# Performance work log

Hardware: AMD Instinct MI355X
Metric: run time of the kernel (lower is better)

Reference implementation:

```python
import jax, jax.numpy as jnp
import numpy as np

BETA = 0.95
THRESH = 1.0
SLOPE = 25.0  # fast_sigmoid surrogate slope

@jax.custom_vjp
def spike(u):
    # Heaviside forward, fast-sigmoid surrogate backward (snntorch.surrogate.fast_sigmoid)
    return (u > 0).astype(u.dtype)

def _spike_fwd(u):
    return spike(u), u

def _spike_bwd(u, g):
    return (g / (SLOPE * jnp.abs(u) + 1.0) ** 2,)

spike.defvjp(_spike_fwd, _spike_bwd)

def setup_inputs() -> dict:
    key = jax.random.key(0)
    ks = jax.random.split(key, 7)
    B, T, D_in, D_h, D_out = 4096, 5, 1024, 4096, 1024
    def lin(kw, kb, fan_in, fan_out):
        bound = 1.0 / np.sqrt(fan_in)
        W = jax.random.uniform(kw, (fan_out, fan_in), jnp.float32, -bound, bound)
        b = jax.random.uniform(kb, (fan_out,), jnp.float32, -bound, bound)
        return W, b
    W1, b1 = lin(ks[0], ks[1], D_in, D_h)
    W2, b2 = lin(ks[2], ks[3], D_h, D_h)
    W3, b3 = lin(ks[4], ks[5], D_h, D_out)
    x = jax.random.normal(ks[6], (B, T, D_in), jnp.float32)
    return {"x": x, "W1": W1, "b1": b1, "W2": W2, "b2": b2, "W3": W3, "b3": b3}

def _lif(cur, mem, spk_prev):
    # snnTorch Leaky, reset_mechanism='subtract': reset uses previous step's (detached) spike
    mem = BETA * mem + cur - jax.lax.stop_gradient(spk_prev) * THRESH
    spk = spike(mem - THRESH)
    return spk, mem

def reference(x, W1, b1, W2, b2, W3, b3):
    B = x.shape[0]
    Dh, Do = W2.shape[0], W3.shape[0]
    z = jnp.zeros((B, Dh), x.dtype)
    zo = jnp.zeros((B, Do), x.dtype)
    init = (z, z, zo, z, z, zo)  # mem1, mem2, mem3, spk1, spk2, spk3

    def step(carry, x_t):
        mem1, mem2, mem3, s1, s2, s3 = carry
        s1, mem1 = _lif(x_t @ W1.T + b1, mem1, s1)
        s2, mem2 = _lif(s1 @ W2.T + b2, mem2, s2)
        s3, mem3 = _lif(s2 @ W3.T + b3, mem3, s3)
        return (mem1, mem2, mem3, s1, s2, s3), s3

    xt = jnp.swapaxes(x, 0, 1)  # [T, B, D_in]
    _, spk3_rec = jax.lax.scan(step, init, xt)
    return spk3_rec.sum(axis=0)  # [B, D_out]
```

## Files before the change

### kernel.cpp

```cpp
#include <hip/hip_runtime.h>
#include <stdint.h>

typedef __attribute__((ext_vector_type(8))) short  short8;
typedef __attribute__((ext_vector_type(4))) float  f32x4;

static constexpr float BETA = 0.95f;
static constexpr unsigned ROWCAP = 64;

__device__ __forceinline__ unsigned short f2bf(float f) {
  uint32_t u = __float_as_uint(f);
  uint32_t r = (u + 0x7fffu + ((u >> 16) & 1u)) >> 16;
  return (unsigned short)r;
}
__device__ __forceinline__ float bf2f(unsigned short s) {
  return __uint_as_float((uint32_t)s << 16);
}

__device__ __forceinline__ void gload16(const void* g, void* l) {
  __builtin_amdgcn_global_load_lds(
      (const __attribute__((address_space(1))) uint32_t*)g,
      (__attribute__((address_space(3))) uint32_t*)l, 16, 0, 0);
}

__global__ void cvt_xt_k(const float* __restrict__ x, unsigned short* __restrict__ xbt, int t) {
  int i = blockIdx.x * blockDim.x + threadIdx.x;
  int k8 = i & 127, b = i >> 7;
  const f32x4* s = (const f32x4*)(x + ((size_t)b * 5 + t) * 1024 + (size_t)k8 * 8);
  f32x4 a = s[0], c = s[1];
  short8 o;
#pragma unroll
  for (int j = 0; j < 4; ++j) { o[j] = (short)f2bf(a[j]); o[4 + j] = (short)f2bf(c[j]); }
  *(short8*)(xbt + (size_t)b * 1024 + (size_t)k8 * 8) = o;
}

__global__ void cvt_w_k(const float* __restrict__ src, unsigned short* __restrict__ dst, int n8) {
  int i = blockIdx.x * blockDim.x + threadIdx.x;
  if (i >= n8) return;
  const f32x4* s = (const f32x4*)src + (size_t)i * 2;
  f32x4 a = s[0], c = s[1];
  short8 o;
#pragma unroll
  for (int j = 0; j < 4; ++j) { o[j] = (short)f2bf(a[j]); o[4 + j] = (short)f2bf(c[j]); }
  *(short8*)(dst + (size_t)i * 8) = o;
}

__global__ void cvt_w3t_k(const float* __restrict__ W3, unsigned short* __restrict__ W3T) {
  __shared__ float tile[32][33];
  const int tx = threadIdx.x & 31, ty = threadIdx.x >> 5;
  const int bc = blockIdx.x * 32, bo = blockIdx.y * 32;
#pragma unroll
  for (int k = 0; k < 4; ++k)
    tile[ty + 8 * k][tx] = W3[(size_t)(bo + ty + 8 * k) * 4096 + bc + tx];
  __syncthreads();
#pragma unroll
  for (int k = 0; k < 4; ++k)
    W3T[(size_t)(bc + ty + 8 * k) * 1024 + bo + tx] = f2bf(tile[tx][ty + 8 * k]);
}

__global__ void zr_k(unsigned int* __restrict__ rcnt) {
  rcnt[blockIdx.x * blockDim.x + threadIdx.x] = 0u;
}

template <bool FIRST, int LAYER>
__global__ __launch_bounds__(512, 2) void gemm_ring(
    const unsigned short* __restrict__ A, const unsigned short* __restrict__ W,
    const float* __restrict__ bias,
    float* __restrict__ mem, unsigned short* __restrict__ sbuf,
    unsigned int* __restrict__ rcnt, unsigned short* __restrict__ rlist,
    int M, int N, int K, int nbn)
{
  __shared__ __align__(16) unsigned short lds[10 * 8192];

  const int tid  = threadIdx.x;
  const int lane = tid & 63;
  const int wid  = tid >> 6;
  const int wr = wid >> 2, wc = wid & 3;

  const int nwg = gridDim.x;
  const int cpx = nwg >> 3;
  const int bid = blockIdx.x;
  const int swz = (bid & 7) * cpx + (bid >> 3);
  const int bm = swz / nbn, bn = swz % nbn;
  const int bmr = bm * 256, bnr = bn * 256;

  const int l15 = lane & 15, l7 = lane & 7, lk = lane >> 4;
  const int aoff0 = l15 * 64 + ((lk)     ^ l7) * 8;
  const int aoff1 = l15 * 64 + ((4 + lk) ^ l7) * 8;
  const int bhoff = (wc & 1) * 4096;

  const int srs = lane >> 3;
  const int sgc = (lane & 7) ^ srs;
  const int ldst = wid * 1024;

  const unsigned short* gAt = A + (size_t)(bmr + wid * 16 + srs) * K + sgc * 8;
  const unsigned short* gBt = W + (size_t)(bnr + wid * 16 + srs) * K + sgc * 8;
  const size_t rK8   = (size_t)8 * K;
  const size_t rK128 = (size_t)128 * K;

  auto stA = [&](int slot, int hh, int kt) {
    const unsigned short* g = gAt + (size_t)hh * rK128 + (size_t)kt * 64;
    unsigned short* d = &lds[slot * 8192 + ldst];
    gload16(g, d);
    gload16(g + rK8, d + 512);
  };
  auto stB = [&](int slot, int hh, int kt) {
    const unsigned short* g = gBt + (size_t)hh * rK128 + (size_t)kt * 64;
    unsigned short* d = &lds[slot * 8192 + ldst];
    gload16(g, d);
    gload16(g + rK8, d + 512);
  };

  f32x4 acc[8][4];
#pragma unroll
  for (int m = 0; m < 8; ++m)
#pragma unroll
    for (int n = 0; n < 4; ++n) acc[m][n] = (f32x4){0.f, 0.f, 0.f, 0.f};

  const int nkt = K >> 6;

  stA(0, 0, 0); stA(1, 1, 0); stB(2, 0, 0); stB(3, 1, 0);
  if (nkt > 1) {
    stA(4, 0, 1); stA(5, 1, 1);
    asm volatile("s_waitcnt vmcnt(4)" ::: "memory");
  } else {
    asm volatile("s_waitcnt vmcnt(0)" ::: "memory");
  }
  asm volatile("s_barrier");
  __builtin_amdgcn_sched_barrier(0);

  int sb = 0;
  for (int t = 0; t < nkt; ++t) {
    int sA = sb + wr;             if (sA >= 10) sA -= 10;
    int sBs = sb + 2 + (wc >> 1); if (sBs >= 10) sBs -= 10;
    const unsigned short* ab = &lds[sA * 8192];
    const unsigned short* bb = &lds[sBs * 8192] + bhoff;
    const bool p1 = (t + 1 < nkt), p2 = (t + 2 < nkt);
    int s6 = sb + 6; if (s6 >= 10) s6 -= 10;
    int s7 = sb + 7; if (s7 >= 10) s7 -= 10;
    int s8 = sb + 8; if (s8 >= 10) s8 -= 10;
    int s9 = sb + 9; if (s9 >= 10) s9 -= 10;

    if (p1) { stB(s6, 0, t + 1); stB(s7, 1, t + 1); }
    if (p2) { stA(s8, 0, t + 2); stA(s9, 1, t + 2); }

    short8 a0[4], b0[4], a1[4], a2[4], b2[4], a3[4];
#pragma unroll
    for (int m = 0; m < 4; ++m) a0[m] = *(const short8*)(ab + m * 1024 + aoff0);
#pragma unroll
    for (int n = 0; n < 4; ++n) b0[n] = *(const short8*)(bb + n * 1024 + aoff0);
#pragma unroll
    for (int m = 0; m < 4; ++m) a1[m] = *(const short8*)(ab + (4 + m) * 1024 + aoff0);
#pragma unroll
    for (int m = 0; m < 4; ++m) a2[m] = *(const short8*)(ab + m * 1024 + aoff1);
#pragma unroll
    for (int n = 0; n < 4; ++n) b2[n] = *(const short8*)(bb + n * 1024 + aoff1);
#pragma unroll
    for (int m = 0; m < 4; ++m) a3[m] = *(const short8*)(ab + (4 + m) * 1024 + aoff1);
    __builtin_amdgcn_sched_barrier(0);

#pragma unroll
    for (int m = 0; m < 4; ++m)
#pragma unroll
      for (int n = 0; n < 4; ++n)
        acc[m][n] = __builtin_amdgcn_mfma_f32_16x16x32_bf16(a0[m], b0[n], acc[m][n], 0, 0, 0);
#pragma unroll
    for (int m = 0; m < 4; ++m)
#pragma unroll
      for (int n = 0; n < 4; ++n)
        acc[4 + m][n] = __builtin_amdgcn_mfma_f32_16x16x32_bf16(a1[m], b0[n], acc[4 + m][n], 0, 0, 0);
#pragma unroll
    for (int m = 0; m < 4; ++m)
#pragma unroll
      for (int n = 0; n < 4; ++n)
        acc[m][n] = __builtin_amdgcn_mfma_f32_16x16x32_bf16(a2[m], b2[n], acc[m][n], 0, 0, 0);
#pragma unroll
    for (int m = 0; m < 4; ++m)
#pragma unroll
      for (int n = 0; n < 4; ++n)
        acc[4 + m][n] = __builtin_amdgcn_mfma_f32_16x16x32_bf16(a3[m], b2[n], acc[4 + m][n], 0, 0, 0);

    if (p2)      asm volatile("s_waitcnt vmcnt(4)" ::: "memory");
    else if (p1) asm volatile("s_waitcnt vmcnt(0)" ::: "memory");
    asm volatile("s_barrier");
    __builtin_amdgcn_sched_barrier(0);

    sb += 4; if (sb >= 10) sb -= 10;
  }

  const int crow0 = bmr + wr * 128;
  const int ccol0 = bnr + wc * 64;
  float bcol[4];
#pragma unroll
  for (int n = 0; n < 4; ++n) bcol[n] = bias[ccol0 + n * 16 + l15];
#pragma unroll
  for (int m = 0; m < 8; ++m) {
#pragma unroll
    for (int n = 0; n < 4; ++n) {
      const int col = ccol0 + n * 16 + l15;
#pragma unroll
      for (int j = 0; j < 4; ++j) {
        const int row = crow0 + m * 16 + lk * 4 + j;
        const size_t idx = (size_t)row * N + col;
        const float curv = acc[m][n][j] + bcol[n];
        const float mold = FIRST ? 0.f : mem[idx];
        const float sprv = FIRST ? 0.f : bf2f(sbuf[idx]);
        const float mnew = BETA * mold + curv - sprv;
        mem[idx] = mnew;
        const float s = (mnew - 1.0f) > 0.f ? 1.f : 0.f;
        sbuf[idx] = f2bf(s);
        if (LAYER == 2) {
          if (s != 0.f) {
            unsigned int slot = atomicAdd(&rcnt[row], 1u);
            if (slot < ROWCAP) rlist[(size_t)row * ROWCAP + slot] = (unsigned short)col;
          }
        }
      }
    }
  }
}

template <bool FIRST>
__global__ void lif3_k(const float* __restrict__ b3,
                       const unsigned int* __restrict__ rcnt,
                       const unsigned short* __restrict__ rlist,
                       const unsigned short* __restrict__ s2,
                       const unsigned short* __restrict__ W3T,
                       float* __restrict__ mem3, unsigned short* __restrict__ s3,
                       float* __restrict__ out) {
  const int i = blockIdx.x * blockDim.x + threadIdx.x;
  const int r = i >> 8, o0 = (i & 255) * 4;
  const size_t idx = (size_t)r * 1024 + o0;

  const unsigned int cnt = rcnt[r];
  f32x4 cur = (f32x4){0.f, 0.f, 0.f, 0.f};
  if (cnt <= ROWCAP) {
    for (unsigned int e = 0; e < cnt; ++e) {
      const unsigned int c = rlist[(size_t)r * ROWCAP + e];
      const ushort4 wv = *(const ushort4*)(W3T + (size_t)c * 1024 + o0);
      cur[0] += bf2f(wv.x); cur[1] += bf2f(wv.y);
      cur[2] += bf2f(wv.z); cur[3] += bf2f(wv.w);
    }
  } else {
    for (int c = 0; c < 4096; ++c) {
      if (s2[(size_t)r * 4096 + c] != 0) {
        const ushort4 wv = *(const ushort4*)(W3T + (size_t)c * 1024 + o0);
        cur[0] += bf2f(wv.x); cur[1] += bf2f(wv.y);
        cur[2] += bf2f(wv.z); cur[3] += bf2f(wv.w);
      }
    }
  }

  const f32x4 bb = *(const f32x4*)(b3 + o0);
  f32x4 mold, sp, ov;
  if (FIRST) {
    mold = (f32x4){0.f, 0.f, 0.f, 0.f};
    sp   = (f32x4){0.f, 0.f, 0.f, 0.f};
  } else {
    mold = *(const f32x4*)(mem3 + idx);
    const ushort4 spv = *(const ushort4*)(s3 + idx);
    sp = (f32x4){bf2f(spv.x), bf2f(spv.y), bf2f(spv.z), bf2f(spv.w)};
    ov = *(const f32x4*)(out + idx);
  }
  f32x4 mnew, sv;
#pragma unroll
  for (int j = 0; j < 4; ++j) {
    mnew[j] = BETA * mold[j] + (cur[j] + bb[j]) - sp[j];
    sv[j] = (mnew[j] - 1.0f) > 0.f ? 1.f : 0.f;
    ov[j] = FIRST ? sv[j] : ov[j] + sv[j];
  }
  *(f32x4*)(mem3 + idx) = mnew;
  ushort4 so = {f2bf(sv[0]), f2bf(sv[1]), f2bf(sv[2]), f2bf(sv[3])};
  *(ushort4*)(s3 + idx) = so;
  *(f32x4*)(out + idx) = ov;
}

extern "C" void kernel_launch(void* const* d_in, const int* in_sizes, int n_in,
                              void* d_out, int out_size, void* d_ws, size_t ws_size,
                              hipStream_t stream)
{
  const float* x  = (const float*)d_in[0];
  const float* W1 = (const float*)d_in[1];
  const float* b1 = (const float*)d_in[2];
  const float* W2 = (const float*)d_in[3];
  const float* b2 = (const float*)d_in[4];
  const float* W3 = (const float*)d_in[5];
  const float* b3 = (const float*)d_in[6];
  float* out = (float*)d_out;

  char* p = (char*)d_ws;
  auto wsalloc = [&](size_t bytes) { char* r = p; p += (bytes + 255) & ~(size_t)255; return r; };
  unsigned short* xbt  = (unsigned short*)wsalloc((size_t)4096 * 1024 * 2);
  unsigned short* W1b  = (unsigned short*)wsalloc((size_t)4096 * 1024 * 2);
  unsigned short* W2b  = (unsigned short*)wsalloc((size_t)4096 * 4096 * 2);
  unsigned short* W3T  = (unsigned short*)wsalloc((size_t)4096 * 1024 * 2);
  unsigned short* s1   = (unsigned short*)wsalloc((size_t)4096 * 4096 * 2);
  unsigned short* s2   = (unsigned short*)wsalloc((size_t)4096 * 4096 * 2);
  unsigned short* s3   = (unsigned short*)wsalloc((size_t)4096 * 1024 * 2);
  float* mem1 = (float*)wsalloc((size_t)4096 * 4096 * 4);
  float* mem2 = (float*)wsalloc((size_t)4096 * 4096 * 4);
  float* mem3 = (float*)wsalloc((size_t)4096 * 1024 * 4);
  unsigned int*   rcnt  = (unsigned int*)wsalloc((size_t)4096 * 4);
  unsigned short* rlist = (unsigned short*)wsalloc((size_t)4096 * ROWCAP * 2);

  cvt_w_k<<<dim3(4096 * 1024 / 8 / 256), dim3(256), 0, stream>>>(W1, W1b, 4096 * 1024 / 8);
  cvt_w_k<<<dim3(4096 * 4096 / 8 / 256), dim3(256), 0, stream>>>(W2, W2b, 4096 * 4096 / 8);
  cvt_w3t_k<<<dim3(128, 32), dim3(256), 0, stream>>>(W3, W3T);

  const dim3 blk(512), blkE(256);
  const dim3 g12(256);
  const dim3 gX(2048), gE(4096), gZ(16);

#define STEP(T, FIRSTV)                                                                         \
  cvt_xt_k<<<gX, blkE, 0, stream>>>(x, xbt, T);                                                 \
  gemm_ring<FIRSTV, 1><<<g12, blk, 0, stream>>>(xbt, W1b, b1, mem1, s1, nullptr, nullptr,       \
                                                4096, 4096, 1024, 16);                          \
  zr_k<<<gZ, blkE, 0, stream>>>(rcnt);                                                          \
  gemm_ring<FIRSTV, 2><<<g12, blk, 0, stream>>>(s1, W2b, b2, mem2, s2, rcnt, rlist,             \
                                                4096, 4096, 4096, 16);                          \
  lif3_k<FIRSTV><<<gE, blkE, 0, stream>>>(b3, rcnt, rlist, s2, W3T, mem3, s3, out)

  STEP(0, true);
  STEP(1, false);
  STEP(2, false);
  STEP(3, false);
  STEP(4, false);
#undef STEP
}
```

Baseline: 1.733 ms.

## Shrink GEMM tile to 256x128 with K-step 32 and raise occupancy

Restructures the layer-1/2 GEMM from 256x256 tiles with K-step 64 to 256x128 tiles with K-step 32. The LDS ring slots are halved, launch bounds ask for 4 blocks per CU, and the grid doubles to 512 blocks. The ring schedule, swizzle and fragment loads are rewritten to match. The aim is better CU coverage and more latency hiding through occupancy, at the cost of lower arithmetic intensity per tile, more global traffic and more barriers per unit of work.

```diff
diff --git a/kernel.cpp b/kernel.cpp
--- a/kernel.cpp
+++ b/kernel.cpp
@@ -62,14 +62,14 @@
 }
 
 template <bool FIRST, int LAYER>
-__global__ __launch_bounds__(512, 2) void gemm_ring(
+__global__ __launch_bounds__(512, 4) void gemm_ring(
     const unsigned short* __restrict__ A, const unsigned short* __restrict__ W,
     const float* __restrict__ bias,
     float* __restrict__ mem, unsigned short* __restrict__ sbuf,
     unsigned int* __restrict__ rcnt, unsigned short* __restrict__ rlist,
     int M, int N, int K, int nbn)
 {
-  __shared__ __align__(16) unsigned short lds[10 * 8192];
+  __shared__ __align__(16) unsigned short lds[10 * 4096];
 
   const int tid  = threadIdx.x;
   const int lane = tid & 63;
@@ -81,47 +81,37 @@
   const int bid = blockIdx.x;
   const int swz = (bid & 7) * cpx + (bid >> 3);
   const int bm = swz / nbn, bn = swz % nbn;
-  const int bmr = bm * 256, bnr = bn * 256;
-
-  const int l15 = lane & 15, l7 = lane & 7, lk = lane >> 4;
-  const int aoff0 = l15 * 64 + ((lk)     ^ l7) * 8;
-  const int aoff1 = l15 * 64 + ((4 + lk) ^ l7) * 8;
-  const int bhoff = (wc & 1) * 4096;
-
-  const int srs = lane >> 3;
-  const int sgc = (lane & 7) ^ srs;
-  const int ldst = wid * 1024;
-
-  const unsigned short* gAt = A + (size_t)(bmr + wid * 16 + srs) * K + sgc * 8;
-  const unsigned short* gBt = W + (size_t)(bnr + wid * 16 + srs) * K + sgc * 8;
-  const size_t rK8   = (size_t)8 * K;
+  const int bmr = bm * 256, bnr = bn * 128;
+
+  const int l15 = lane & 15, lk = lane >> 4;
+  const int aoff = l15 * 32 + ((lk ^ (l15 & 3)) << 3);
+
+  const int srow = tid >> 2;
+  const int lg   = (tid & 3) ^ (srow & 3);
+
+  const unsigned short* gA0 = A + (size_t)(bmr + srow) * K + lg * 8;
+  const unsigned short* gB0 = W + (size_t)(bnr + srow) * K + lg * 8;
   const size_t rK128 = (size_t)128 * K;
 
   auto stA = [&](int slot, int hh, int kt) {
-    const unsigned short* g = gAt + (size_t)hh * rK128 + (size_t)kt * 64;
-    unsigned short* d = &lds[slot * 8192 + ldst];
-    gload16(g, d);
-    gload16(g + rK8, d + 512);
+    gload16(gA0 + (size_t)hh * rK128 + (size_t)kt * 32, &lds[slot * 4096 + tid * 8]);
   };
-  auto stB = [&](int slot, int hh, int kt) {
-    const unsigned short* g = gBt + (size_t)hh * rK128 + (size_t)kt * 64;
-    unsigned short* d = &lds[slot * 8192 + ldst];
-    gload16(g, d);
-    gload16(g + rK8, d + 512);
+  auto stB = [&](int slot, int kt) {
+    gload16(gB0 + (size_t)kt * 32, &lds[slot * 4096 + tid * 8]);
   };
 
-  f32x4 acc[8][4];
+  f32x4 acc[8][2];
 #pragma unroll
   for (int m = 0; m < 8; ++m)
 #pragma unroll
-    for (int n = 0; n < 4; ++n) acc[m][n] = (f32x4){0.f, 0.f, 0.f, 0.f};
-
-  const int nkt = K >> 6;
-
-  stA(0, 0, 0); stA(1, 1, 0); stB(2, 0, 0); stB(3, 1, 0);
+    for (int n = 0; n < 2; ++n) acc[m][n] = (f32x4){0.f, 0.f, 0.f, 0.f};
+
+  const int nkt = K >> 5;
+
+  stA(0, 0, 0); stA(1, 1, 0); stB(2, 0);
   if (nkt > 1) {
-    stA(4, 0, 1); stA(5, 1, 1);
-    asm volatile("s_waitcnt vmcnt(4)" ::: "memory");
+    stA(3, 0, 1); stA(4, 1, 1);
+    asm volatile("s_waitcnt vmcnt(2)" ::: "memory");
   } else {
     asm volatile("s_waitcnt vmcnt(0)" ::: "memory");
   }
@@ -130,72 +120,53 @@
 
   int sb = 0;
   for (int t = 0; t < nkt; ++t) {
-    int sA = sb + wr;             if (sA >= 10) sA -= 10;
-    int sBs = sb + 2 + (wc >> 1); if (sBs >= 10) sBs -= 10;
-    const unsigned short* ab = &lds[sA * 8192];
-    const unsigned short* bb = &lds[sBs * 8192] + bhoff;
+    int sA = sb + wr;  if (sA >= 10) sA -= 10;
+    int sB = sb + 2;   if (sB >= 10) sB -= 10;
+    const unsigned short* ab = &lds[sA * 4096];
+    const unsigned short* bb = &lds[sB * 4096] + wc * 1024;
     const bool p1 = (t + 1 < nkt), p2 = (t + 2 < nkt);
+    int s5 = sb + 5; if (s5 >= 10) s5 -= 10;
     int s6 = sb + 6; if (s6 >= 10) s6 -= 10;
     int s7 = sb + 7; if (s7 >= 10) s7 -= 10;
-    int s8 = sb + 8; if (s8 >= 10) s8 -= 10;
-    int s9 = sb + 9; if (s9 >= 10) s9 -= 10;
-
-    if (p1) { stB(s6, 0, t + 1); stB(s7, 1, t + 1); }
-    if (p2) { stA(s8, 0, t + 2); stA(s9, 1, t + 2); }
-
-    short8 a0[4], b0[4], a1[4], a2[4], b2[4], a3[4];
-#pragma unroll
-    for (int m = 0; m < 4; ++m) a0[m] = *(const short8*)(ab + m * 1024 + aoff0);
-#pragma unroll
-    for (int n = 0; n < 4; ++n) b0[n] = *(const short8*)(bb + n * 1024 + aoff0);
-#pragma unroll
-    for (int m = 0; m < 4; ++m) a1[m] = *(const short8*)(ab + (4 + m) * 1024 + aoff0);
-#pragma unroll
-    for (int m = 0; m < 4; ++m) a2[m] = *(const short8*)(ab + m * 1024 + aoff1);
-#pragma unroll
-    for (int n = 0; n < 4; ++n) b2[n] = *(const short8*)(bb + n * 1024 + aoff1);
-#pragma unroll
-    for (int m = 0; m < 4; ++m) a3[m] = *(const short8*)(ab + (4 + m) * 1024 + aoff1);
-    __builtin_amdgcn_sched_barrier(0);
-
+
+    if (p1) stB(s5, t + 1);
+    if (p2) { stA(s6, 0, t + 2); stA(s7, 1, t + 2); }
+
+    short8 bfr[2], af[4];
+#pragma unroll
+    for (int n = 0; n < 2; ++n) bfr[n] = *(const short8*)(bb + n * 512 + aoff);
+#pragma unroll
+    for (int m = 0; m < 4; ++m) af[m] = *(const short8*)(ab + m * 512 + aoff);
 #pragma unroll
     for (int m = 0; m < 4; ++m)
 #pragma unroll
-      for (int n = 0; n < 4; ++n)
-        acc[m][n] = __builtin_amdgcn_mfma_f32_16x16x32_bf16(a0[m], b0[n], acc[m][n], 0, 0, 0);
+      for (int n = 0; n < 2; ++n)
+        acc[m][n] = __builtin_amdgcn_mfma_f32_16x16x32_bf16(af[m], bfr[n], acc[m][n], 0, 0, 0);
+#pragma unroll
+    for (int m = 0; m < 4; ++m) af[m] = *(const short8*)(ab + (4 + m) * 512 + aoff);
 #pragma unroll
     for (int m = 0; m < 4; ++m)
 #pragma unroll
-      for (int n = 0; n < 4; ++n)
-        acc[4 + m][n] = __builtin_amdgcn_mfma_f32_16x16x32_bf16(a1[m], b0[n], acc[4 + m][n], 0, 0, 0);
-#pragma unroll
-    for (int m = 0; m < 4; ++m)
-#pragma unroll
-      for (int n = 0; n < 4; ++n)
-        acc[m][n] = __builtin_amdgcn_mfma_f32_16x16x32_bf16(a2[m], b2[n], acc[m][n], 0, 0, 0);
-#pragma unroll
-    for (int m = 0; m < 4; ++m)
-#pragma unroll
-      for (int n = 0; n < 4; ++n)
-        acc[4 + m][n] = __builtin_amdgcn_mfma_f32_16x16x32_bf16(a3[m], b2[n], acc[4 + m][n], 0, 0, 0);
-
-    if (p2)      asm volatile("s_waitcnt vmcnt(4)" ::: "memory");
+      for (int n = 0; n < 2; ++n)
+        acc[4 + m][n] = __builtin_amdgcn_mfma_f32_16x16x32_bf16(af[m], bfr[n], acc[4 + m][n], 0, 0, 0);
+
+    if (p2)      asm volatile("s_waitcnt vmcnt(2)" ::: "memory");
     else if (p1) asm volatile("s_waitcnt vmcnt(0)" ::: "memory");
     asm volatile("s_barrier");
     __builtin_amdgcn_sched_barrier(0);
 
-    sb += 4; if (sb >= 10) sb -= 10;
+    sb += 3; if (sb >= 10) sb -= 10;
   }
 
   const int crow0 = bmr + wr * 128;
-  const int ccol0 = bnr + wc * 64;
-  float bcol[4];
-#pragma unroll
-  for (int n = 0; n < 4; ++n) bcol[n] = bias[ccol0 + n * 16 + l15];
+  const int ccol0 = bnr + wc * 32;
+  float bcol[2];
+#pragma unroll
+  for (int n = 0; n < 2; ++n) bcol[n] = bias[ccol0 + n * 16 + l15];
 #pragma unroll
   for (int m = 0; m < 8; ++m) {
 #pragma unroll
-    for (int n = 0; n < 4; ++n) {
+    for (int n = 0; n < 2; ++n) {
       const int col = ccol0 + n * 16 + l15;
 #pragma unroll
       for (int j = 0; j < 4; ++j) {
@@ -307,16 +278,16 @@
   cvt_w3t_k<<<dim3(128, 32), dim3(256), 0, stream>>>(W3, W3T);
 
   const dim3 blk(512), blkE(256);
-  const dim3 g12(256);
+  const dim3 g12(512);
   const dim3 gX(2048), gE(4096), gZ(16);
 
 #define STEP(T, FIRSTV)                                                                         \
   cvt_xt_k<<<gX, blkE, 0, stream>>>(x, xbt, T);                                                 \
   gemm_ring<FIRSTV, 1><<<g12, blk, 0, stream>>>(xbt, W1b, b1, mem1, s1, nullptr, nullptr,       \
-                                                4096, 4096, 1024, 16);                          \
+                                                4096, 4096, 1024, 32);                          \
   zr_k<<<gZ, blkE, 0, stream>>>(rcnt);                                                          \
   gemm_ring<FIRSTV, 2><<<g12, blk, 0, stream>>>(s1, W2b, b2, mem2, s2, rcnt, rlist,             \
-                                                4096, 4096, 4096, 16);                          \
+                                                4096, 4096, 4096, 32);                          \
   lif3_k<FIRSTV><<<gE, blkE, 0, stream>>>(b3, rcnt, rlist, s2, W3T, mem3, s3, out)
 
   STEP(0, true);
```

Result: faster. 1.653 ms (-4.6%).
